# Performance work log

Hardware: AMD Instinct MI355X
Metric: run time of the kernel (lower is better)

## Reference

```python
import jax, jax.numpy as jnp
import numpy as np

B, T, D, H = 4, 2048, 512, 8
DK = D // H


def setup_inputs() -> dict:
    key0 = jax.random.key(0)
    ks = jax.random.split(key0, 16)
    s = 1.0 / np.sqrt(D)
    inp = {
        "query": jax.random.normal(ks[0], (B, T, D), jnp.float32),
        "key": jax.random.normal(ks[1], (B, T, D), jnp.float32),
        "value": jax.random.normal(ks[2], (B, T, D), jnp.float32),
        "mask": jnp.ones((B, 1, T), jnp.int32),
        "pos_emb": jax.random.normal(ks[3], (1, T, D), jnp.float32),
        "Wq": jax.random.normal(ks[4], (D, D), jnp.float32) * s,
        "bq": jnp.zeros((D,), jnp.float32),
        "Wk": jax.random.normal(ks[5], (D, D), jnp.float32) * s,
        "bk": jnp.zeros((D,), jnp.float32),
        "Wv": jax.random.normal(ks[6], (D, D), jnp.float32) * s,
        "bv": jnp.zeros((D,), jnp.float32),
        "Wo": jax.random.normal(ks[7], (D, D), jnp.float32) * s,
        "bo": jnp.zeros((D,), jnp.float32),
        "Wp": jax.random.normal(ks[8], (D, D), jnp.float32) * s,  # linear_pos, no bias
        "pos_bias_u": jax.random.normal(ks[9], (H, DK), jnp.float32) * 0.05,
        "pos_bias_v": jax.random.normal(ks[10], (H, DK), jnp.float32) * 0.05,
    }
    return inp


def reference(query, key, value, mask, pos_emb, Wq, bq, Wk, bk, Wv, bv, Wo, bo, Wp, pos_bias_u, pos_bias_v):
    b, t1, d = query.shape
    h, dk = pos_bias_u.shape
    # projections -> (b, t, h, dk)
    q = (query @ Wq.T + bq).reshape(b, t1, h, dk)
    k = (key @ Wk.T + bk).reshape(b, -1, h, dk)
    v = (value @ Wv.T + bv).reshape(b, -1, h, dk)
    # positional projection (n_batch_pos == 1): (t2, h, dk)
    p = (pos_emb @ Wp.T).reshape(pos_emb.shape[0], -1, h, dk)[0]
    # content score (a+c) and position score (b+d); NOTE: this repo's forward
    # does not apply rel_shift -- matrix_bd is used directly.
    matrix_ac = jnp.einsum("bthd,bshd->bhts", q + pos_bias_u, k)
    matrix_bd = jnp.einsum("bthd,shd->bhts", q + pos_bias_v, p)
    scores = (matrix_ac + matrix_bd) / np.sqrt(dk)
    # mask: (b, 1, t2) -> (b, 1, 1, t2); masked where mask == 0
    m = (mask[:, None, :, :] == 0)
    scores = jnp.where(m, -jnp.inf, scores)
    attn = jax.nn.softmax(scores, axis=-1)
    attn = jnp.where(m, 0.0, attn)
    x = jnp.einsum("bhts,bshd->bthd", attn, v).reshape(b, t1, h * dk)
    return x @ Wo.T + bo
```

## Files before the change

kernel.cpp:

```cpp
#include <hip/hip_runtime.h>

typedef __bf16 bf16;
typedef __attribute__((ext_vector_type(8))) __bf16 bf16x8;
typedef __attribute__((ext_vector_type(4))) __bf16 bf16x4;
typedef __attribute__((ext_vector_type(4))) float f32x4;
typedef __attribute__((ext_vector_type(4))) short s4;

#define NB 4
#define NT 2048
#define ND 512
#define NH 8
#define NDK 64
#define GAMMA 0.1803368801111204f
#define LTS 152

#define OFF_XQ 0ull
#define OFF_XK 4194304ull
#define OFF_XV 8388608ull
#define OFF_XP 12582912ull
#define OFF_WQ 13631488ull
#define OFF_WK 13893632ull
#define OFF_WV 14155776ull
#define OFF_WP 14417920ull
#define OFF_WO 14680064ull
#define OFF_QU 14942208ull
#define OFF_QV 19136512ull
#define OFF_KB 23330816ull
#define OFF_VT 27525120ull
#define OFF_PB 31719424ull
#define OFF_OA OFF_XQ

static __device__ __forceinline__ f32x4 mfma16b(s4 a, s4 b, f32x4 c) {
#if __has_builtin(__builtin_amdgcn_mfma_f32_16x16x16bf16_1k)
  return __builtin_amdgcn_mfma_f32_16x16x16bf16_1k(a, b, c, 0, 0, 0);
#else
  f32x4 d;
  asm("v_mfma_f32_16x16x16_bf16 %0, %1, %2, %3"
      : "=v"(d)
      : "v"(a), "v"(b), "v"(c));
  return d;
#endif
}

__global__ __launch_bounds__(256) void convert_bf16(
    const float* __restrict__ q, const float* __restrict__ k,
    const float* __restrict__ v, const float* __restrict__ p,
    const float* __restrict__ wq, const float* __restrict__ wk,
    const float* __restrict__ wv, const float* __restrict__ wp,
    const float* __restrict__ wo, bf16* __restrict__ dst) {
  int bid = blockIdx.x;
  const float* src;
  size_t doff;
  if (bid < 2048) { src = q; doff = OFF_XQ; }
  else if (bid < 4096) { src = k; doff = OFF_XK; bid -= 2048; }
  else if (bid < 6144) { src = v; doff = OFF_XV; bid -= 4096; }
  else if (bid < 6656) { src = p; doff = OFF_XP; bid -= 6144; }
  else if (bid < 6784) { src = wq; doff = OFF_WQ; bid -= 6656; }
  else if (bid < 6912) { src = wk; doff = OFF_WK; bid -= 6784; }
  else if (bid < 7040) { src = wv; doff = OFF_WV; bid -= 6912; }
  else if (bid < 7168) { src = wp; doff = OFF_WP; bid -= 7040; }
  else { src = wo; doff = OFF_WO; bid -= 7168; }
  size_t base = (size_t)bid * 2048 + threadIdx.x * 8;
  float4 x0 = *(const float4*)(src + base);
  float4 x1 = *(const float4*)(src + base + 4);
  bf16x8 o;
  o[0] = (bf16)x0.x; o[1] = (bf16)x0.y; o[2] = (bf16)x0.z; o[3] = (bf16)x0.w;
  o[4] = (bf16)x1.x; o[5] = (bf16)x1.y; o[6] = (bf16)x1.z; o[7] = (bf16)x1.w;
  *(bf16x8*)(dst + doff + base) = o;
}

__device__ __forceinline__ void flush_tile(const bf16* LT, bf16* dst, int bm,
                                           int bn, int tid, bool isP) {
#pragma unroll
  for (int i = 0; i < 8; i++) {
    int chunk = tid + i * 256;
    int mm = chunk >> 4, c8 = (chunk & 15) * 8;
    bf16x8 vv = *(const bf16x8*)&LT[mm * LTS + c8];
    int n = bn + c8, h = n >> 6, d = n & 63;
    int gm = bm + mm;
    size_t gidx;
    if (isP)
      gidx = ((size_t)h * NT + gm) * NDK + d;
    else
      gidx = ((size_t)((gm >> 11) * NH + h) * NT + (gm & 2047)) * NDK + d;
    *(bf16x8*)(dst + gidx) = vv;
  }
}

__global__ __launch_bounds__(256) void proj_fused(
    const bf16* __restrict__ Xq, const bf16* __restrict__ Xk,
    const bf16* __restrict__ Xv, const bf16* __restrict__ Xp,
    const bf16* __restrict__ wq, const bf16* __restrict__ wk,
    const bf16* __restrict__ wv, const bf16* __restrict__ wp,
    const float* __restrict__ bq, const float* __restrict__ bk,
    const float* __restrict__ bv, const float* __restrict__ pu,
    const float* __restrict__ pv, bf16* __restrict__ Qu, bf16* __restrict__ Qv,
    bf16* __restrict__ Kb, bf16* __restrict__ Vt, bf16* __restrict__ Pb) {
  __shared__ bf16 smem[2][128][76];

  const int bid = blockIdx.x;
  const int mode = (bid >= 768) ? 3 : (bid >> 8);
  const int idx = (mode == 3) ? bid - 768 : (bid & 255);
  const int bm = (idx >> 2) * 128, bn = (idx & 3) * 128;

  const bf16* X;
  const bf16* W;
  if (mode == 0) { X = Xq; W = wq; }
  else if (mode == 1) { X = Xk; W = wk; }
  else if (mode == 2) { X = Xv; W = wv; }
  else { X = Xp; W = wp; }

  const int tid = threadIdx.x;
  const int l = tid & 63, w = tid >> 6;
  const int q = l >> 4, ln = l & 15;
  const int wm = (w >> 1) * 64, wn = (w & 1) * 64;

  f32x4 acc[4][4];
#pragma unroll
  for (int i = 0; i < 4; i++)
#pragma unroll
    for (int j = 0; j < 4; j++) acc[i][j] = (f32x4){0.f, 0.f, 0.f, 0.f};

  const int srow = tid >> 3, scol = (tid & 7) * 8;
  const size_t abase = (size_t)(bm + srow) * 512 + scol;
  const size_t bbase = (size_t)(bn + srow) * 512 + scol;

  bf16x8 ar[4], br[4];
#pragma unroll
  for (int i = 0; i < 4; i++) {
    ar[i] = *(const bf16x8*)(X + abase + (size_t)i * 32 * 512);
    br[i] = *(const bf16x8*)(W + bbase + (size_t)i * 32 * 512);
  }

  for (int k0 = 0; k0 < 512; k0 += 64) {
    __syncthreads();
#pragma unroll
    for (int i = 0; i < 4; i++) {
      *(bf16x8*)&smem[0][srow + i * 32][scol] = ar[i];
      *(bf16x8*)&smem[1][srow + i * 32][scol] = br[i];
    }
    if (k0 + 64 < 512) {
#pragma unroll
      for (int i = 0; i < 4; i++) {
        ar[i] = *(const bf16x8*)(X + abase + k0 + 64 + (size_t)i * 32 * 512);
        br[i] = *(const bf16x8*)(W + bbase + k0 + 64 + (size_t)i * 32 * 512);
      }
    }
    __syncthreads();
#pragma unroll
    for (int kc = 0; kc < 2; kc++) {
      bf16x8 af[4], bfr[4];
#pragma unroll
      for (int rt = 0; rt < 4; rt++)
        af[rt] = *(const bf16x8*)&smem[0][wm + rt * 16 + ln][kc * 32 + q * 8];
#pragma unroll
      for (int ct = 0; ct < 4; ct++)
        bfr[ct] = *(const bf16x8*)&smem[1][wn + ct * 16 + ln][kc * 32 + q * 8];
      if (mode == 2) {
#pragma unroll
        for (int rt = 0; rt < 4; rt++)
#pragma unroll
          for (int ct = 0; ct < 4; ct++)
            acc[rt][ct] = __builtin_amdgcn_mfma_f32_16x16x32_bf16(
                af[rt], bfr[ct], acc[rt][ct], 0, 0, 0);
      } else {
#pragma unroll
        for (int rt = 0; rt < 4; rt++)
#pragma unroll
          for (int ct = 0; ct < 4; ct++)
            acc[rt][ct] = __builtin_amdgcn_mfma_f32_16x16x32_bf16(
                bfr[ct], af[rt], acc[rt][ct], 0, 0, 0);
      }
    }
  }

  bf16* LT = &smem[0][0][0];

  if (mode == 2) {
    __syncthreads();
#pragma unroll
    for (int ct = 0; ct < 4; ct++) {
      const int n = bn + wn + ct * 16 + ln;
      const float bvn = bv[n];
#pragma unroll
      for (int rt = 0; rt < 4; rt++) {
        bf16x4 t4;
#pragma unroll
        for (int r = 0; r < 4; r++) t4[r] = (bf16)(acc[rt][ct][r] + bvn);
        *(bf16x4*)&LT[(wn + ct * 16 + ln) * LTS + wm + rt * 16 + q * 4] = t4;
      }
    }
    __syncthreads();
    const int b = bm >> 11, tb = bm & 2047;
#pragma unroll
    for (int i = 0; i < 8; i++) {
      int chunk = tid + i * 256;
      int nn = chunk >> 4, m8 = (chunk & 15) * 8;
      int n = bn + nn, h = n >> 6, d = n & 63;
      size_t gidx = (((size_t)(b * NH + h)) * NDK + d) * NT + tb + m8;
      *(bf16x8*)(Vt + gidx) = *(const bf16x8*)&LT[nn * LTS + m8];
    }
    return;
  }

  const int mloc = wm + ln;
  const int nloc = wn + q * 4;

  if (mode == 0) {
    float4 addu4[4], addv4[4];
#pragma unroll
    for (int ct = 0; ct < 4; ct++) {
      int n0 = bn + nloc + ct * 16;
      float4 bb = *(const float4*)(bq + n0);
      float4 uu = *(const float4*)(pu + n0);
      float4 vv = *(const float4*)(pv + n0);
      addu4[ct] = make_float4(bb.x + uu.x, bb.y + uu.y, bb.z + uu.z, bb.w + uu.w);
      addv4[ct] = make_float4(bb.x + vv.x, bb.y + vv.y, bb.z + vv.z, bb.w + vv.w);
    }
    __syncthreads();
#pragma unroll
    for (int rt = 0; rt < 4; rt++)
#pragma unroll
      for (int ct = 0; ct < 4; ct++) {
        const float* au = &addu4[ct].x;
        bf16x4 t4;
#pragma unroll
        for (int r = 0; r < 4; r++)
          t4[r] = (bf16)((acc[rt][ct][r] + au[r]) * GAMMA);
        *(bf16x4*)&LT[(mloc + rt * 16) * LTS + nloc + ct * 16] = t4;
      }
    __syncthreads();
    flush_tile(LT, Qu, bm, bn, tid, false);
    __syncthreads();
#pragma unroll
    for (int rt = 0; rt < 4; rt++)
#pragma unroll
      for (int ct = 0; ct < 4; ct++) {
        const float* av = &addv4[ct].x;
        bf16x4 t4;
#pragma unroll
        for (int r = 0; r < 4; r++)
          t4[r] = (bf16)((acc[rt][ct][r] + av[r]) * GAMMA);
        *(bf16x4*)&LT[(mloc + rt * 16) * LTS + nloc + ct * 16] = t4;
      }
    __syncthreads();
    flush_tile(LT, Qv, bm, bn, tid, false);
    return;
  }

  {
    float4 bb4[4];
#pragma unroll
    for (int ct = 0; ct < 4; ct++) {
      int n0 = bn + nloc + ct * 16;
      bb4[ct] = (mode == 1) ? *(const float4*)(bk + n0)
                            : make_float4(0.f, 0.f, 0.f, 0.f);
    }
    __syncthreads();
#pragma unroll
    for (int rt = 0; rt < 4; rt++)
#pragma unroll
      for (int ct = 0; ct < 4; ct++) {
        const float* bbp = &bb4[ct].x;
        bf16x4 t4;
#pragma unroll
        for (int r = 0; r < 4; r++) t4[r] = (bf16)(acc[rt][ct][r] + bbp[r]);
        *(bf16x4*)&LT[(mloc + rt * 16) * LTS + nloc + ct * 16] = t4;
      }
    __syncthreads();
    flush_tile(LT, (mode == 1) ? Kb : Pb, bm, bn, tid, mode == 3);
  }
}

__global__ __launch_bounds__(512) void flash(
    const bf16* __restrict__ Qu, const bf16* __restrict__ Qv,
    const bf16* __restrict__ Kb, const bf16* __restrict__ Pb,
    const bf16* __restrict__ Vt, const int* __restrict__ mask,
    bf16* __restrict__ Oa) {
  __shared__ bf16 sK[64][136];
  __shared__ bf16 sVt[64][72];
  __shared__ float sbias[64];

  const int tid = threadIdx.x;
  const int l = tid & 63, wv = tid >> 6;
  const int q = l >> 4, ln = l & 15;
  const int t0 = blockIdx.x * 256;
  const int bh = blockIdx.y;
  const int b = bh >> 3;

  bf16x8 qf[2][4];
#pragma unroll
  for (int tt = 0; tt < 2; tt++) {
    const size_t qrow = (((size_t)bh) * NT + t0 + wv * 32 + tt * 16 + ln) * NDK;
    qf[tt][0] = *(const bf16x8*)(Qu + qrow + q * 8);
    qf[tt][1] = *(const bf16x8*)(Qu + qrow + 32 + q * 8);
    qf[tt][2] = *(const bf16x8*)(Qv + qrow + q * 8);
    qf[tt][3] = *(const bf16x8*)(Qv + qrow + 32 + q * 8);
  }

  int okacc = 1;
  for (int i = tid; i < NT; i += 512) okacc &= (mask[b * NT + i] != 0);
  const int allones = __syncthreads_and(okacc);

  float lsum[2] = {0.f, 0.f};
  f32x4 O[2][4];
#pragma unroll
  for (int tt = 0; tt < 2; tt++)
#pragma unroll
    for (int dt = 0; dt < 4; dt++) O[tt][dt] = (f32x4){0.f, 0.f, 0.f, 0.f};

  const bf16* Krow = Kb + ((size_t)bh) * NT * NDK;
  const bf16* Prow = Pb + ((size_t)(bh & 7)) * NT * NDK;
  const bf16* Vrow = Vt + ((size_t)bh) * NDK * NT;

  const int krow = tid >> 4, kcc = tid & 15;
  const int vrow = tid >> 3, vcol = (tid & 7) * 8;
  const bf16* kpsrc = (kcc < 8) ? (Krow + kcc * 8) : (Prow + (kcc - 8) * 8);

  bf16x8 rk[2], rv;
#pragma unroll
  for (int i = 0; i < 2; i++)
    rk[i] = *(const bf16x8*)(kpsrc + (size_t)(krow + i * 32) * NDK);
  rv = *(const bf16x8*)(Vrow + (size_t)vrow * NT + vcol);

  for (int s0 = 0; s0 < NT; s0 += 64) {
    __syncthreads();
#pragma unroll
    for (int i = 0; i < 2; i++) *(bf16x8*)&sK[krow + i * 32][kcc * 8] = rk[i];
    *(bf16x8*)&sVt[vrow][vcol] = rv;
    if (s0 + 64 < NT) {
#pragma unroll
      for (int i = 0; i < 2; i++)
        rk[i] =
            *(const bf16x8*)(kpsrc + (size_t)(s0 + 64 + krow + i * 32) * NDK);
      rv = *(const bf16x8*)(Vrow + (size_t)vrow * NT + s0 + 64 + vcol);
    }
    if (!allones && tid < 64)
      sbias[tid] = mask[b * NT + s0 + tid] ? 0.f : -1e30f;
    __syncthreads();

    f32x4 ST[2][4];
#pragma unroll
    for (int ct = 0; ct < 4; ct++) {
      ST[0][ct] = (f32x4){0.f, 0.f, 0.f, 0.f};
      ST[1][ct] = (f32x4){0.f, 0.f, 0.f, 0.f};
#pragma unroll
      for (int kc = 0; kc < 4; kc++) {
        bf16x8 kf = *(const bf16x8*)&sK[ct * 16 + ln][kc * 32 + q * 8];
        ST[0][ct] = __builtin_amdgcn_mfma_f32_16x16x32_bf16(kf, qf[0][kc],
                                                            ST[0][ct], 0, 0, 0);
        ST[1][ct] = __builtin_amdgcn_mfma_f32_16x16x32_bf16(kf, qf[1][kc],
                                                            ST[1][ct], 0, 0, 0);
      }
    }
    if (!allones) {
#pragma unroll
      for (int ct = 0; ct < 4; ct++) {
        float4 bb = *(const float4*)&sbias[ct * 16 + q * 4];
#pragma unroll
        for (int tt = 0; tt < 2; tt++) {
          ST[tt][ct][0] += bb.x;
          ST[tt][ct][1] += bb.y;
          ST[tt][ct][2] += bb.z;
          ST[tt][ct][3] += bb.w;
        }
      }
    }
#pragma unroll
    for (int ct = 0; ct < 4; ct++) {
      s4 pa[2];
#pragma unroll
      for (int tt = 0; tt < 2; tt++) {
        unsigned u0 =
            __builtin_bit_cast(unsigned, __builtin_amdgcn_exp2f(ST[tt][ct][0]));
        unsigned u1 =
            __builtin_bit_cast(unsigned, __builtin_amdgcn_exp2f(ST[tt][ct][1]));
        unsigned u2 =
            __builtin_bit_cast(unsigned, __builtin_amdgcn_exp2f(ST[tt][ct][2]));
        unsigned u3 =
            __builtin_bit_cast(unsigned, __builtin_amdgcn_exp2f(ST[tt][ct][3]));
        lsum[tt] += __builtin_bit_cast(float, u0 & 0xffff0000u) +
                    __builtin_bit_cast(float, u1 & 0xffff0000u) +
                    __builtin_bit_cast(float, u2 & 0xffff0000u) +
                    __builtin_bit_cast(float, u3 & 0xffff0000u);
        uint2 pk;
        pk.x = (u0 >> 16) | (u1 & 0xffff0000u);
        pk.y = (u2 >> 16) | (u3 & 0xffff0000u);
        pa[tt] = __builtin_bit_cast(s4, pk);
      }
#pragma unroll
      for (int dt = 0; dt < 4; dt++) {
        s4 vb = *(const s4*)&sVt[dt * 16 + ln][ct * 16 + q * 4];
        O[0][dt] = mfma16b(pa[0], vb, O[0][dt]);
        O[1][dt] = mfma16b(pa[1], vb, O[1][dt]);
      }
    }
  }

#pragma unroll
  for (int tt = 0; tt < 2; tt++) {
    float s = lsum[tt];
    s += __shfl_xor(s, 16);
    s += __shfl_xor(s, 32);
#pragma unroll
    for (int r = 0; r < 4; r++) {
      float dr = __shfl(s, q * 4 + r);
      float inv = (dr > 0.f) ? 1.f / dr : 0.f;
      int t = t0 + wv * 32 + tt * 16 + q * 4 + r;
      size_t base = (((size_t)b * NT + t) * NH + (bh & 7)) * NDK;
#pragma unroll
      for (int dt = 0; dt < 4; dt++)
        Oa[base + dt * 16 + ln] = (bf16)(O[tt][dt][r] * inv);
    }
  }
}

__global__ __launch_bounds__(256) void out_gemm(const bf16* __restrict__ A,
                                                const bf16* __restrict__ W,
                                                const float* __restrict__ bias,
                                                float* __restrict__ out) {
  __shared__ bf16 sA[128][72];
  __shared__ bf16 sB[64][72];

  const int tid = threadIdx.x;
  const int l = tid & 63, w = tid >> 6;
  const int q = l >> 4, ln = l & 15;
  const int wm = (w >> 1) * 64, wn = (w & 1) * 32;
  const int bm = blockIdx.x * 128, bn = blockIdx.y * 64;

  f32x4 acc[4][2];
#pragma unroll
  for (int i = 0; i < 4; i++)
#pragma unroll
    for (int j = 0; j < 2; j++) acc[i][j] = (f32x4){0.f, 0.f, 0.f, 0.f};

  const int srow = tid >> 3, scol = (tid & 7) * 8;
  const size_t abase = (size_t)(bm + srow) * 512 + scol;
  const size_t bbase = (size_t)(bn + srow) * 512 + scol;

  bf16x8 ar[4], br[2];
#pragma unroll
  for (int i = 0; i < 4; i++)
    ar[i] = *(const bf16x8*)(A + abase + (size_t)i * 32 * 512);
#pragma unroll
  for (int i = 0; i < 2; i++)
    br[i] = *(const bf16x8*)(W + bbase + (size_t)i * 32 * 512);

  for (int k0 = 0; k0 < 512; k0 += 64) {
    __syncthreads();
#pragma unroll
    for (int i = 0; i < 4; i++) *(bf16x8*)&sA[srow + i * 32][scol] = ar[i];
#pragma unroll
    for (int i = 0; i < 2; i++) *(bf16x8*)&sB[srow + i * 32][scol] = br[i];
    if (k0 + 64 < 512) {
#pragma unroll
      for (int i = 0; i < 4; i++)
        ar[i] = *(const bf16x8*)(A + abase + k0 + 64 + (size_t)i * 32 * 512);
#pragma unroll
      for (int i = 0; i < 2; i++)
        br[i] = *(const bf16x8*)(W + bbase + k0 + 64 + (size_t)i * 32 * 512);
    }
    __syncthreads();
#pragma unroll
    for (int kc = 0; kc < 2; kc++) {
      bf16x8 af[4], bfr[2];
#pragma unroll
      for (int rt = 0; rt < 4; rt++)
        af[rt] = *(const bf16x8*)&sA[wm + rt * 16 + ln][kc * 32 + q * 8];
#pragma unroll
      for (int ct = 0; ct < 2; ct++)
        bfr[ct] = *(const bf16x8*)&sB[wn + ct * 16 + ln][kc * 32 + q * 8];
#pragma unroll
      for (int rt = 0; rt < 4; rt++)
#pragma unroll
        for (int ct = 0; ct < 2; ct++)
          acc[rt][ct] = __builtin_amdgcn_mfma_f32_16x16x32_bf16(
              af[rt], bfr[ct], acc[rt][ct], 0, 0, 0);
    }
  }

#pragma unroll
  for (int rt = 0; rt < 4; rt++)
#pragma unroll
    for (int ct = 0; ct < 2; ct++) {
      const int n = bn + wn + ct * 16 + ln;
      const float bias_n = bias[n];
#pragma unroll
      for (int r = 0; r < 4; r++) {
        const int m = bm + wm + rt * 16 + q * 4 + r;
        out[(size_t)m * 512 + n] = acc[rt][ct][r] + bias_n;
      }
    }
}

extern "C" void kernel_launch(void* const* d_in, const int* in_sizes, int n_in,
                              void* d_out, int out_size, void* d_ws,
                              size_t ws_size, hipStream_t stream) {
  const float* query = (const float*)d_in[0];
  const float* key = (const float*)d_in[1];
  const float* value = (const float*)d_in[2];
  const int* mask = (const int*)d_in[3];
  const float* pos = (const float*)d_in[4];
  const float* Wq = (const float*)d_in[5];
  const float* bq = (const float*)d_in[6];
  const float* Wk = (const float*)d_in[7];
  const float* bk = (const float*)d_in[8];
  const float* Wv = (const float*)d_in[9];
  const float* bv = (const float*)d_in[10];
  const float* Wo = (const float*)d_in[11];
  const float* bo = (const float*)d_in[12];
  const float* Wp = (const float*)d_in[13];
  const float* pu = (const float*)d_in[14];
  const float* pv = (const float*)d_in[15];
  float* out = (float*)d_out;

  bf16* ws = (bf16*)d_ws;
  dim3 blk(256);
  convert_bf16<<<dim3(7296), blk, 0, stream>>>(query, key, value, pos, Wq, Wk,
                                               Wv, Wp, Wo, ws);
  proj_fused<<<dim3(832), blk, 0, stream>>>(
      ws + OFF_XQ, ws + OFF_XK, ws + OFF_XV, ws + OFF_XP, ws + OFF_WQ,
      ws + OFF_WK, ws + OFF_WV, ws + OFF_WP, bq, bk, bv, pu, pv, ws + OFF_QU,
      ws + OFF_QV, ws + OFF_KB, ws + OFF_VT, ws + OFF_PB);
  flash<<<dim3(8, 32), dim3(512), 0, stream>>>(ws + OFF_QU, ws + OFF_QV,
                                               ws + OFF_KB, ws + OFF_PB,
                                               ws + OFF_VT, mask, ws + OFF_OA);
  out_gemm<<<dim3(64, 8), blk, 0, stream>>>(ws + OFF_OA, ws + OFF_WO, bo, out);
}
```

Measured before the change: 223.9 us.

## Fuse activation fp32-to-bf16 conversion into projection GEMM loads

Stops pre-converting the query/key/value/pos activations to bf16 in a separate kernel. The projection GEMM now loads fp32 activations directly and converts them in registers before the shared-memory store, and the conversion kernel only handles weights. The Q epilogue also writes Qu and Qv in a single flush pass, deriving Qv from Qu plus a per-column delta. This saves a full read-write pass over about 14M elements, at the cost of doubled global load width per GEMM tile and a small extra bf16 rounding step on Qv.

```diff
diff --git a/kernel.cpp b/kernel.cpp
--- a/kernel.cpp
+++ b/kernel.cpp
@@ -14,10 +14,6 @@
 #define GAMMA 0.1803368801111204f
 #define LTS 152
 
-#define OFF_XQ 0ull
-#define OFF_XK 4194304ull
-#define OFF_XV 8388608ull
-#define OFF_XP 12582912ull
 #define OFF_WQ 13631488ull
 #define OFF_WK 13893632ull
 #define OFF_WV 14155776ull
@@ -28,7 +24,7 @@
 #define OFF_KB 23330816ull
 #define OFF_VT 27525120ull
 #define OFF_PB 31719424ull
-#define OFF_OA OFF_XQ
+#define OFF_OA 0ull
 
 static __device__ __forceinline__ f32x4 mfma16b(s4 a, s4 b, f32x4 c) {
 #if __has_builtin(__builtin_amdgcn_mfma_f32_16x16x16bf16_1k)
@@ -42,25 +38,20 @@
 #endif
 }
 
-__global__ __launch_bounds__(256) void convert_bf16(
-    const float* __restrict__ q, const float* __restrict__ k,
-    const float* __restrict__ v, const float* __restrict__ p,
+__global__ __launch_bounds__(256) void convert_w(
     const float* __restrict__ wq, const float* __restrict__ wk,
     const float* __restrict__ wv, const float* __restrict__ wp,
     const float* __restrict__ wo, bf16* __restrict__ dst) {
   int bid = blockIdx.x;
+  const int m = bid >> 7, sub = bid & 127;
   const float* src;
-  size_t doff;
-  if (bid < 2048) { src = q; doff = OFF_XQ; }
-  else if (bid < 4096) { src = k; doff = OFF_XK; bid -= 2048; }
-  else if (bid < 6144) { src = v; doff = OFF_XV; bid -= 4096; }
-  else if (bid < 6656) { src = p; doff = OFF_XP; bid -= 6144; }
-  else if (bid < 6784) { src = wq; doff = OFF_WQ; bid -= 6656; }
-  else if (bid < 6912) { src = wk; doff = OFF_WK; bid -= 6784; }
-  else if (bid < 7040) { src = wv; doff = OFF_WV; bid -= 6912; }
-  else if (bid < 7168) { src = wp; doff = OFF_WP; bid -= 7040; }
-  else { src = wo; doff = OFF_WO; bid -= 7168; }
-  size_t base = (size_t)bid * 2048 + threadIdx.x * 8;
+  if (m == 0) src = wq;
+  else if (m == 1) src = wk;
+  else if (m == 2) src = wv;
+  else if (m == 3) src = wp;
+  else src = wo;
+  size_t doff = OFF_WQ + (size_t)m * 262144;
+  size_t base = (size_t)sub * 2048 + threadIdx.x * 8;
   float4 x0 = *(const float4*)(src + base);
   float4 x1 = *(const float4*)(src + base + 4);
   bf16x8 o;
@@ -88,8 +79,8 @@
 }
 
 __global__ __launch_bounds__(256) void proj_fused(
-    const bf16* __restrict__ Xq, const bf16* __restrict__ Xk,
-    const bf16* __restrict__ Xv, const bf16* __restrict__ Xp,
+    const float* __restrict__ Xq, const float* __restrict__ Xk,
+    const float* __restrict__ Xv, const float* __restrict__ Xp,
     const bf16* __restrict__ wq, const bf16* __restrict__ wk,
     const bf16* __restrict__ wv, const bf16* __restrict__ wp,
     const float* __restrict__ bq, const float* __restrict__ bk,
@@ -103,7 +94,7 @@
   const int idx = (mode == 3) ? bid - 768 : (bid & 255);
   const int bm = (idx >> 2) * 128, bn = (idx & 3) * 128;
 
-  const bf16* X;
+  const float* X;
   const bf16* W;
   if (mode == 0) { X = Xq; W = wq; }
   else if (mode == 1) { X = Xk; W = wk; }
@@ -125,10 +116,12 @@
   const size_t abase = (size_t)(bm + srow) * 512 + scol;
   const size_t bbase = (size_t)(bn + srow) * 512 + scol;
 
-  bf16x8 ar[4], br[4];
+  float4 arf[4][2];
+  bf16x8 br[4];
 #pragma unroll
   for (int i = 0; i < 4; i++) {
-    ar[i] = *(const bf16x8*)(X + abase + (size_t)i * 32 * 512);
+    arf[i][0] = *(const float4*)(X + abase + (size_t)i * 32 * 512);
+    arf[i][1] = *(const float4*)(X + abase + (size_t)i * 32 * 512 + 4);
     br[i] = *(const bf16x8*)(W + bbase + (size_t)i * 32 * 512);
   }
 
@@ -136,13 +129,21 @@
     __syncthreads();
 #pragma unroll
     for (int i = 0; i < 4; i++) {
-      *(bf16x8*)&smem[0][srow + i * 32][scol] = ar[i];
+      bf16x8 a8;
+      a8[0] = (bf16)arf[i][0].x; a8[1] = (bf16)arf[i][0].y;
+      a8[2] = (bf16)arf[i][0].z; a8[3] = (bf16)arf[i][0].w;
+      a8[4] = (bf16)arf[i][1].x; a8[5] = (bf16)arf[i][1].y;
+      a8[6] = (bf16)arf[i][1].z; a8[7] = (bf16)arf[i][1].w;
+      *(bf16x8*)&smem[0][srow + i * 32][scol] = a8;
       *(bf16x8*)&smem[1][srow + i * 32][scol] = br[i];
     }
     if (k0 + 64 < 512) {
 #pragma unroll
       for (int i = 0; i < 4; i++) {
-        ar[i] = *(const bf16x8*)(X + abase + k0 + 64 + (size_t)i * 32 * 512);
+        arf[i][0] =
+            *(const float4*)(X + abase + k0 + 64 + (size_t)i * 32 * 512);
+        arf[i][1] =
+            *(const float4*)(X + abase + k0 + 64 + (size_t)i * 32 * 512 + 4);
         br[i] = *(const bf16x8*)(W + bbase + k0 + 64 + (size_t)i * 32 * 512);
       }
     }
@@ -207,15 +208,14 @@
   const int nloc = wn + q * 4;
 
   if (mode == 0) {
-    float4 addu4[4], addv4[4];
+    float4 addu4[4];
 #pragma unroll
     for (int ct = 0; ct < 4; ct++) {
       int n0 = bn + nloc + ct * 16;
       float4 bb = *(const float4*)(bq + n0);
       float4 uu = *(const float4*)(pu + n0);
-      float4 vv = *(const float4*)(pv + n0);
-      addu4[ct] = make_float4(bb.x + uu.x, bb.y + uu.y, bb.z + uu.z, bb.w + uu.w);
-      addv4[ct] = make_float4(bb.x + vv.x, bb.y + vv.y, bb.z + vv.z, bb.w + vv.w);
+      addu4[ct] =
+          make_float4(bb.x + uu.x, bb.y + uu.y, bb.z + uu.z, bb.w + uu.w);
     }
     __syncthreads();
 #pragma unroll
@@ -230,21 +230,35 @@
         *(bf16x4*)&LT[(mloc + rt * 16) * LTS + nloc + ct * 16] = t4;
       }
     __syncthreads();
-    flush_tile(LT, Qu, bm, bn, tid, false);
-    __syncthreads();
-#pragma unroll
-    for (int rt = 0; rt < 4; rt++)
-#pragma unroll
-      for (int ct = 0; ct < 4; ct++) {
-        const float* av = &addv4[ct].x;
-        bf16x4 t4;
-#pragma unroll
-        for (int r = 0; r < 4; r++)
-          t4[r] = (bf16)((acc[rt][ct][r] + av[r]) * GAMMA);
-        *(bf16x4*)&LT[(mloc + rt * 16) * LTS + nloc + ct * 16] = t4;
-      }
-    __syncthreads();
-    flush_tile(LT, Qv, bm, bn, tid, false);
+    const int c8 = (tid & 15) * 8;
+    float delta8[8];
+    {
+      int n0 = bn + c8;
+      float4 u0 = *(const float4*)(pu + n0);
+      float4 u1 = *(const float4*)(pu + n0 + 4);
+      float4 v0 = *(const float4*)(pv + n0);
+      float4 v1 = *(const float4*)(pv + n0 + 4);
+      delta8[0] = (v0.x - u0.x) * GAMMA; delta8[1] = (v0.y - u0.y) * GAMMA;
+      delta8[2] = (v0.z - u0.z) * GAMMA; delta8[3] = (v0.w - u0.w) * GAMMA;
+      delta8[4] = (v1.x - u1.x) * GAMMA; delta8[5] = (v1.y - u1.y) * GAMMA;
+      delta8[6] = (v1.z - u1.z) * GAMMA; delta8[7] = (v1.w - u1.w) * GAMMA;
+    }
+    const int n = bn + c8, h = n >> 6, d = n & 63;
+#pragma unroll
+    for (int i = 0; i < 8; i++) {
+      int chunk = tid + i * 256;
+      int mm = chunk >> 4;
+      bf16x8 qu8 = *(const bf16x8*)&LT[mm * LTS + c8];
+      bf16x8 qv8;
+#pragma unroll
+      for (int j = 0; j < 8; j++)
+        qv8[j] = (bf16)((float)qu8[j] + delta8[j]);
+      int gm = bm + mm;
+      size_t gidx =
+          ((size_t)((gm >> 11) * NH + h) * NT + (gm & 2047)) * NDK + d;
+      *(bf16x8*)(Qu + gidx) = qu8;
+      *(bf16x8*)(Qv + gidx) = qv8;
+    }
     return;
   }
 
@@ -516,12 +530,11 @@
 
   bf16* ws = (bf16*)d_ws;
   dim3 blk(256);
-  convert_bf16<<<dim3(7296), blk, 0, stream>>>(query, key, value, pos, Wq, Wk,
-                                               Wv, Wp, Wo, ws);
+  convert_w<<<dim3(640), blk, 0, stream>>>(Wq, Wk, Wv, Wp, Wo, ws);
   proj_fused<<<dim3(832), blk, 0, stream>>>(
-      ws + OFF_XQ, ws + OFF_XK, ws + OFF_XV, ws + OFF_XP, ws + OFF_WQ,
-      ws + OFF_WK, ws + OFF_WV, ws + OFF_WP, bq, bk, bv, pu, pv, ws + OFF_QU,
-      ws + OFF_QV, ws + OFF_KB, ws + OFF_VT, ws + OFF_PB);
+      query, key, value, pos, ws + OFF_WQ, ws + OFF_WK, ws + OFF_WV,
+      ws + OFF_WP, bq, bk, bv, pu, pv, ws + OFF_QU, ws + OFF_QV, ws + OFF_KB,
+      ws + OFF_VT, ws + OFF_PB);
   flash<<<dim3(8, 32), dim3(512), 0, stream>>>(ws + OFF_QU, ws + OFF_QV,
                                                ws + OFF_KB, ws + OFF_PB,
                                                ws + OFF_VT, mask, ws + OFF_OA);
```

Result: faster. 213.2 us (-4.8%).
